# Optimization experiments

Measured on AMD Instinct MI355X. Metric: run time of the kernel, lower is better.

The kernel has to match this reference:

```python
import jax, jax.numpy as jnp
import numpy as np

B, K, F_DIM, H_DIM, HEADS = 512, 17, 256, 256, 4
N = B * K           # 8704 flattened nodes
E = 139264          # edges (avg degree 16)
NEG_SLOPE = 0.2


def setup_inputs() -> dict:
    key = jax.random.key(0)
    ks = jax.random.split(key, 12)
    s_in = 1.0 / np.sqrt(F_DIM)
    s_hid = 1.0 / np.sqrt(H_DIM)
    return {
        "kpt_feature": jax.random.normal(ks[0], (B, K, F_DIM), jnp.float32),
        "edge_index": jax.random.randint(ks[1], (2, E), 0, N, jnp.int64),
        # conv1: F_DIM -> HEADS x H_DIM, concat=False (mean)
        "W1": jax.random.normal(ks[2], (F_DIM, HEADS * H_DIM), jnp.float32) * s_in,
        "a_src1": jax.random.normal(ks[3], (HEADS, H_DIM), jnp.float32) * s_hid,
        "a_dst1": jax.random.normal(ks[4], (HEADS, H_DIM), jnp.float32) * s_hid,
        "b1": jnp.zeros((H_DIM,), jnp.float32),
        # conv2: H_DIM -> HEADS x F_DIM, concat=False (mean)
        "W2": jax.random.normal(ks[5], (H_DIM, HEADS * F_DIM), jnp.float32) * s_hid,
        "a_src2": jax.random.normal(ks[6], (HEADS, F_DIM), jnp.float32) * s_in,
        "a_dst2": jax.random.normal(ks[7], (HEADS, F_DIM), jnp.float32) * s_in,
        "b2": jnp.zeros((F_DIM,), jnp.float32),
    }


def gat_conv(x, src, dst, W, a_src, a_dst, bias):
    # x: [N, Fin]; src/dst: [E'] (self-loops included); W: [Fin, H*C]
    n = x.shape[0]
    heads, c = a_src.shape
    h = (x @ W).reshape(n, heads, c)                       # [N,H,C]
    alpha_src = jnp.einsum("nhc,hc->nh", h, a_src)         # [N,H]
    alpha_dst = jnp.einsum("nhc,hc->nh", h, a_dst)
    e = jax.nn.leaky_relu(alpha_src[src] + alpha_dst[dst], NEG_SLOPE)  # [E',H]
    # segment softmax over incoming edges of each destination node
    emax = jax.ops.segment_max(e, dst, num_segments=n)
    emax = jnp.where(jnp.isfinite(emax), emax, 0.0)
    ex = jnp.exp(e - emax[dst])
    denom = jax.ops.segment_sum(ex, dst, num_segments=n)
    alpha = ex / denom[dst]                                # [E',H]
    msg = alpha[:, :, None] * h[src]                       # [E',H,C]
    out = jax.ops.segment_sum(msg, dst, num_segments=n)    # [N,H,C]
    return out.mean(axis=1) + bias                         # concat=False -> mean


def reference(kpt_feature, edge_index, W1, a_src1, a_dst1, b1, W2, a_src2, a_dst2, b2):
    b, k, f = kpt_feature.shape
    n = b * k
    x = kpt_feature.reshape(n, f)
    loop = jnp.arange(n, dtype=edge_index.dtype)
    src = jnp.concatenate([edge_index[0], loop])  # PyG add_self_loops=True
    dst = jnp.concatenate([edge_index[1], loop])
    x = gat_conv(x, src, dst, W1, a_src1, a_dst1, b1)
    x = jax.nn.relu(x)
    x = gat_conv(x, src, dst, W2, a_src2, a_dst2, b2)
    return x.reshape(b, k, f)
```

## Files before the change

### kernel.cpp

```cpp
#include <hip/hip_runtime.h>
#include <hip/hip_fp16.h>
#include <math.h>

#define NNODES 8704
#define FDIM   256
#define HD     1024
#define NEDGE  139264
#define EPLUS  (NEDGE + NNODES)
#define NEG_SLOPE 0.2f
#define DEGCAP 64
#define LDSK   40

typedef _Float16 f16x8 __attribute__((ext_vector_type(8)));
typedef _Float16 f16x4 __attribute__((ext_vector_type(4)));
typedef _Float16 f16x2 __attribute__((ext_vector_type(2)));
typedef float    f32x4 __attribute__((ext_vector_type(4)));

__device__ __forceinline__ float lrelu(float v) { return v >= 0.f ? v : NEG_SLOPE * v; }

__global__ __launch_bounds__(256) void prep_pvec(const float* __restrict__ W1,
                                                 const float* __restrict__ as1,
                                                 const float* __restrict__ ad1,
                                                 const float* __restrict__ W2,
                                                 const float* __restrict__ as2,
                                                 const float* __restrict__ ad2,
                                                 float* __restrict__ pbuf,
                                                 int* __restrict__ cnt,
                                                 float* __restrict__ alphasB ) {
    const int b = blockIdx.x;
    const int t = threadIdx.x;
    for (int i = b * 256 + t; i < NNODES; i += 16 * 256) cnt[i] = 0;
    for (int i = b * 256 + t; i < NNODES * 8; i += 16 * 256) alphasB[i] = 0.f;
    __shared__ float a_sh[256];
    const int layer = b >> 3, sd = (b >> 2) & 1, h = b & 3;
    const float* W  = layer ? W2 : W1;
    const float* av = layer ? (sd ? ad2 : as2) : (sd ? ad1 : as1);
    a_sh[t] = av[h * 256 + t];
    __syncthreads();
    float acc = 0.f;
    const float* Wr = W + (size_t)t * 1024 + h * 256;
#pragma unroll 8
    for (int c = 0; c < 256; ++c) acc += Wr[c] * a_sh[c];
    pbuf[b * 256 + t] = acc;
}

__global__ __launch_bounds__(256) void prep_wcat(const float* __restrict__ W1,
                                                 const float* __restrict__ W2,
                                                 _Float16* __restrict__ Wc1,
                                                 _Float16* __restrict__ Wc2) {
    __shared__ float tile[32][33];
    const int k0 = blockIdx.x * 32, o0 = blockIdx.y * 32;
    const int layer = blockIdx.z >> 2, h = blockIdx.z & 3;
    const float* W = layer ? W2 : W1;
    _Float16* Wc   = layer ? Wc2 : Wc1;
    const int t = threadIdx.x;
#pragma unroll
    for (int p = 0; p < 4; ++p) {
        int e = t + p * 256; int kk = e >> 5, oo = e & 31;
        tile[kk][oo] = W[(size_t)(k0 + kk) * 1024 + h * 256 + o0 + oo];
    }
    __syncthreads();
#pragma unroll
    for (int p = 0; p < 4; ++p) {
        int e = t + p * 256; int oo = e >> 5, kk = e & 31;
        Wc[(size_t)(o0 + oo) * 1024 + h * 256 + k0 + kk] = (_Float16)tile[kk][oo];
    }
}

__global__ void edge_scatter(const int* __restrict__ ei, int* __restrict__ cnt,
                             int* __restrict__ csr) {
    int e = blockIdx.x * 256 + threadIdx.x;
    if (e >= EPLUS) return;
    int src, dst;
    if (e < NEDGE) { src = ei[e]; dst = ei[NEDGE + e]; }
    else           { src = dst = e - NEDGE; }
    int slot = atomicAdd(&cnt[dst], 1);
    if (slot < DEGCAP) csr[dst * DEGCAP + slot] = src;
}

__global__ __launch_bounds__(256) void alpha_dots(const float* __restrict__ xf,
                                                  _Float16* __restrict__ xh_out,
                                                  const float* __restrict__ p ,
                                                  float* __restrict__ asrc,
                                                  float* __restrict__ adst) {
    const int wave = threadIdx.x >> 6, l = threadIdx.x & 63;
    const int n = blockIdx.x * 4 + wave;
    float4 pv[8];
#pragma unroll
    for (int v = 0; v < 8; ++v) pv[v] = *(const float4*)(p + v * 256 + l * 4);
    float4 xv = *(const float4*)(xf + (size_t)n * 256 + l * 4);
    f16x4 hv = {(_Float16)xv.x, (_Float16)xv.y, (_Float16)xv.z, (_Float16)xv.w};
    *(f16x4*)(xh_out + (size_t)n * 256 + l * 4) = hv;
    float d[8];
#pragma unroll
    for (int v = 0; v < 8; ++v)
        d[v] = xv.x * pv[v].x + xv.y * pv[v].y + xv.z * pv[v].z + xv.w * pv[v].w;
#pragma unroll
    for (int off = 1; off <= 32; off <<= 1)
#pragma unroll
        for (int v = 0; v < 8; ++v) d[v] += __shfl_xor(d[v], off);
    if (l == 0) {
        *(float4*)(asrc + n * 4) = make_float4(d[0], d[1], d[2], d[3]);
        *(float4*)(adst + n * 4) = make_float4(d[4], d[5], d[6], d[7]);
    }
}

__global__ __launch_bounds__(256) void agg_gather(const _Float16* __restrict__ xh,
                                                  const int* __restrict__ cnt,
                                                  const int* __restrict__ csr,
                                                  const float* __restrict__ asrc,
                                                  const float* __restrict__ adst,
                                                  _Float16* __restrict__ y) {
    __shared__ float wbuf[DEGCAP][4];
    __shared__ int   sbuf[DEGCAP];
    __shared__ float sdinv[4];
    __shared__ float partial[4][4][256];

    const int n = blockIdx.x;
    const int t = threadIdx.x;
    int deg = cnt[n]; if (deg > DEGCAP) deg = DEGCAP;

    if (t < 64) {
        float4 ad = *(const float4*)(adst + n * 4);
        float w0 = 0.f, w1 = 0.f, w2 = 0.f, w3 = 0.f;
        if (t < deg) {
            int src = csr[n * DEGCAP + t];
            sbuf[t] = src;
            float4 as = *(const float4*)(asrc + src * 4);
            w0 = __expf(lrelu(as.x + ad.x));
            w1 = __expf(lrelu(as.y + ad.y));
            w2 = __expf(lrelu(as.z + ad.z));
            w3 = __expf(lrelu(as.w + ad.w));
            wbuf[t][0] = w0; wbuf[t][1] = w1; wbuf[t][2] = w2; wbuf[t][3] = w3;
        }
        float d0 = w0, d1 = w1, d2 = w2, d3 = w3;
#pragma unroll
        for (int off = 32; off >= 1; off >>= 1) {
            d0 += __shfl_xor(d0, off);
            d1 += __shfl_xor(d1, off);
            d2 += __shfl_xor(d2, off);
            d3 += __shfl_xor(d3, off);
        }
        if (t == 0) {
            sdinv[0] = 1.f / d0; sdinv[1] = 1.f / d1;
            sdinv[2] = 1.f / d2; sdinv[3] = 1.f / d3;
        }
    }
    __syncthreads();
    for (int i = t; i < deg * 4; i += 256) wbuf[i >> 2][i & 3] *= sdinv[i & 3];
    __syncthreads();

    const int g = t >> 6, l = t & 63;
    float acc[4][4] = {};
    for (int s = g; s < deg; s += 4) {
        int src = sbuf[s];
        float w0 = wbuf[s][0], w1 = wbuf[s][1], w2 = wbuf[s][2], w3 = wbuf[s][3];
        f16x4 xv = *(const f16x4*)(xh + (size_t)src * 256 + l * 4);
#pragma unroll
        for (int j = 0; j < 4; ++j) {
            float v = (float)xv[j];
            acc[j][0] += w0 * v; acc[j][1] += w1 * v;
            acc[j][2] += w2 * v; acc[j][3] += w3 * v;
        }
    }
#pragma unroll
    for (int j = 0; j < 4; ++j)
#pragma unroll
        for (int h = 0; h < 4; ++h) partial[g][h][l * 4 + j] = acc[j][h];
    __syncthreads();

    if (t < 128) {
#pragma unroll
        for (int h = 0; h < 4; ++h) {
            float v0 = partial[0][h][2*t]   + partial[1][h][2*t]   + partial[2][h][2*t]   + partial[3][h][2*t];
            float v1 = partial[0][h][2*t+1] + partial[1][h][2*t+1] + partial[2][h][2*t+1] + partial[3][h][2*t+1];
            f16x2 o = {(_Float16)v0, (_Float16)v1};
            *(f16x2*)(y + (size_t)n * 1024 + h * 256 + 2 * t) = o;
        }
    }
}

__global__ __launch_bounds__(256) void gemm_out(const _Float16* __restrict__ Y,
                                                const _Float16* __restrict__ Wcatt,
                                                const float* __restrict__ bias,
                                                const float* __restrict__ p2,
                                                _Float16* __restrict__ outH,
                                                float* __restrict__ outF,
                                                float* __restrict__ asrc2,
                                                float* __restrict__ adst2) {
    __shared__ __align__(16) _Float16 As[64 * LDSK];
    __shared__ __align__(16) _Float16 Bs[256 * LDSK];
    __shared__ float p2s[8 * 256];
    const int t    = threadIdx.x;
    const int lane = t & 63;
    const int wave = t >> 6;
    const int wwr = wave >> 1, wwc = wave & 1;
    const int bm = blockIdx.x * 64;
    const int l15 = lane & 15, kb = lane >> 4;

    f32x4 acc[2][8] = {};

    int a_off[2], b_off[8];
#pragma unroll
    for (int i = 0; i < 2; ++i) a_off[i] = (wwr * 32 + i * 16 + l15) * LDSK + kb * 8;
#pragma unroll
    for (int j = 0; j < 8; ++j) b_off[j] = (wwc * 128 + j * 16 + l15) * LDSK + kb * 8;

    for (int k0 = 0; k0 < 1024; k0 += 32) {
        if (k0) __syncthreads();
        {
            int row = t >> 2, g = t & 3;
            f16x8 v = *(const f16x8*)(Y + (size_t)(bm + row) * 1024 + k0 + g * 8);
            *(f16x8*)(&As[row * LDSK + g * 8]) = v;
        }
#pragma unroll
        for (int p = 0; p < 4; ++p) {
            int e = t + p * 256;
            int row = e >> 2, g = e & 3;
            f16x8 v = *(const f16x8*)(Wcatt + (size_t)row * 1024 + k0 + g * 8);
            *(f16x8*)(&Bs[row * LDSK + g * 8]) = v;
        }
        __syncthreads();

        f16x8 af[2], bf[8];
#pragma unroll
        for (int i = 0; i < 2; ++i) af[i] = *(const f16x8*)(&As[a_off[i]]);
#pragma unroll
        for (int j = 0; j < 8; ++j) bf[j] = *(const f16x8*)(&Bs[b_off[j]]);
#pragma unroll
        for (int i = 0; i < 2; ++i)
#pragma unroll
            for (int j = 0; j < 8; ++j)
                acc[i][j] = __builtin_amdgcn_mfma_f32_16x16x32_f16(af[i], bf[j], acc[i][j], 0, 0, 0);
    }

    if (p2) {
#pragma unroll
        for (int v = 0; v < 8; ++v) p2s[v * 256 + t] = p2[v * 256 + t];
    }
    __syncthreads();

#pragma unroll
    for (int i = 0; i < 2; ++i)
#pragma unroll
        for (int q = 0; q < 4; ++q) {
            int row = bm + wwr * 32 + i * 16 + kb * 4 + q;
            float rv[8];
#pragma unroll
            for (int j = 0; j < 8; ++j) {
                int col = wwc * 128 + j * 16 + l15;
                float r = 0.25f * acc[i][j][q] + bias[col];
                rv[j] = r;
                if (outH) outH[(size_t)row * 256 + col] = (_Float16)fmaxf(r, 0.f);
                else      outF[(size_t)row * 256 + col] = r;
            }
            if (p2) {
#pragma unroll
                for (int v = 0; v < 8; ++v) {
                    float ps = 0.f;
#pragma unroll
                    for (int j = 0; j < 8; ++j) {
                        int col = wwc * 128 + j * 16 + l15;
                        ps += fmaxf(rv[j], 0.f) * p2s[v * 256 + col];
                    }
#pragma unroll
                    for (int off = 1; off <= 8; off <<= 1) ps += __shfl_xor(ps, off);
                    if (l15 == 0) {
                        if (v < 4) atomicAdd(&asrc2[row * 4 + v], ps);
                        else       atomicAdd(&adst2[row * 4 + (v - 4)], ps);
                    }
                }
            }
        }
}

extern "C" void kernel_launch(void* const* d_in, const int* in_sizes, int n_in,
                              void* d_out, int out_size, void* d_ws, size_t ws_size,
                              hipStream_t stream) {
    const float* x0  = (const float*)d_in[0];
    const int*   ei  = (const int*)d_in[1];
    const float* W1  = (const float*)d_in[2];
    const float* as1 = (const float*)d_in[3];
    const float* ad1 = (const float*)d_in[4];
    const float* b1  = (const float*)d_in[5];
    const float* W2  = (const float*)d_in[6];
    const float* as2 = (const float*)d_in[7];
    const float* ad2 = (const float*)d_in[8];
    const float* b2  = (const float*)d_in[9];
    float* out = (float*)d_out;

    char* w = (char*)d_ws;
    _Float16* y   = (_Float16*)w; w += (size_t)NNODES * HD * 2;
    _Float16* x0h = (_Float16*)w; w += (size_t)NNODES * FDIM * 2;
    _Float16* x1h = (_Float16*)w; w += (size_t)NNODES * FDIM * 2;
    _Float16* Wc1 = (_Float16*)w; w += (size_t)256 * 1024 * 2;
    _Float16* Wc2 = (_Float16*)w; w += (size_t)256 * 1024 * 2;
    float* pbuf   = (float*)w;    w += 16 * 256 * 4;
    float* asrcA  = (float*)w;    w += NNODES * 4 * 4;
    float* adstA  = (float*)w;    w += NNODES * 4 * 4;
    float* alphasB = (float*)w;   w += NNODES * 8 * 4;
    float* asrcB  = alphasB;
    float* adstB  = alphasB + NNODES * 4;
    int* cnt      = (int*)w;      w += NNODES * 4;
    int* csr      = (int*)w;      w += (size_t)NNODES * DEGCAP * 4;

    const dim3 eb((EPLUS + 255) / 256);
    const dim3 wcat_grid(8, 8, 8);

    prep_pvec<<<16, 256, 0, stream>>>(W1, as1, ad1, W2, as2, ad2, pbuf, cnt, alphasB);
    prep_wcat<<<wcat_grid, 256, 0, stream>>>(W1, W2, Wc1, Wc2);
    edge_scatter<<<eb, 256, 0, stream>>>(ei, cnt, csr);

    alpha_dots<<<NNODES / 4, 256, 0, stream>>>(x0, x0h, pbuf, asrcA, adstA);
    agg_gather<<<NNODES, 256, 0, stream>>>(x0h, cnt, csr, asrcA, adstA, y);
    gemm_out<<<NNODES / 64, 256, 0, stream>>>(y, Wc1, b1, pbuf + 8 * 256, x1h, nullptr, asrcB, adstB);

    agg_gather<<<NNODES, 256, 0, stream>>>(x1h, cnt, csr, asrcB, adstB, y);
    gemm_out<<<NNODES / 64, 256, 0, stream>>>(y, Wc2, b2, nullptr, nullptr, out, nullptr, nullptr);
}
```

Measured before the change: 149.4 us.

## Split output GEMM across column tiles to increase block count

Change the output GEMM tiling from a 64x256 tile per block to 64x64 tiles over a 2D grid, with a deeper K step of 64 and padded LDS rows. This raises the number of blocks so more compute units are occupied. The fused attention-score epilogue now accumulates partial dot products per column block through atomics. The trade-off is redundant reloading of the Y activation tile across the four column blocks and lower MFMA work per LDS load.

```diff
diff --git a/kernel.cpp b/kernel.cpp
--- a/kernel.cpp
+++ b/kernel.cpp
@@ -10,6 +10,7 @@
 #define NEG_SLOPE 0.2f
 #define DEGCAP 64
 #define LDSK   40
+#define LDSK2  72
 
 typedef _Float16 f16x8 __attribute__((ext_vector_type(8)));
 typedef _Float16 f16x4 __attribute__((ext_vector_type(4)));
@@ -188,55 +189,60 @@
                                                 float* __restrict__ outF,
                                                 float* __restrict__ asrc2,
                                                 float* __restrict__ adst2) {
-    __shared__ __align__(16) _Float16 As[64 * LDSK];
-    __shared__ __align__(16) _Float16 Bs[256 * LDSK];
-    __shared__ float p2s[8 * 256];
+    __shared__ __align__(16) _Float16 As[64 * LDSK2];
+    __shared__ __align__(16) _Float16 Bs[64 * LDSK2];
+    __shared__ float p2s[8 * 64];
     const int t    = threadIdx.x;
     const int lane = t & 63;
     const int wave = t >> 6;
     const int wwr = wave >> 1, wwc = wave & 1;
     const int bm = blockIdx.x * 64;
+    const int bn = blockIdx.y * 64;
     const int l15 = lane & 15, kb = lane >> 4;
 
-    f32x4 acc[2][8] = {};
-
-    int a_off[2], b_off[8];
-#pragma unroll
-    for (int i = 0; i < 2; ++i) a_off[i] = (wwr * 32 + i * 16 + l15) * LDSK + kb * 8;
-#pragma unroll
-    for (int j = 0; j < 8; ++j) b_off[j] = (wwc * 128 + j * 16 + l15) * LDSK + kb * 8;
-
-    for (int k0 = 0; k0 < 1024; k0 += 32) {
+    f32x4 acc[2][2] = {};
+
+    int a_off[2], b_off[2];
+#pragma unroll
+    for (int i = 0; i < 2; ++i) a_off[i] = (wwr * 32 + i * 16 + l15) * LDSK2 + kb * 8;
+#pragma unroll
+    for (int j = 0; j < 2; ++j) b_off[j] = (wwc * 32 + j * 16 + l15) * LDSK2 + kb * 8;
+
+    for (int k0 = 0; k0 < 1024; k0 += 64) {
         if (k0) __syncthreads();
-        {
-            int row = t >> 2, g = t & 3;
-            f16x8 v = *(const f16x8*)(Y + (size_t)(bm + row) * 1024 + k0 + g * 8);
-            *(f16x8*)(&As[row * LDSK + g * 8]) = v;
-        }
-#pragma unroll
-        for (int p = 0; p < 4; ++p) {
+#pragma unroll
+        for (int p = 0; p < 2; ++p) {
             int e = t + p * 256;
-            int row = e >> 2, g = e & 3;
-            f16x8 v = *(const f16x8*)(Wcatt + (size_t)row * 1024 + k0 + g * 8);
-            *(f16x8*)(&Bs[row * LDSK + g * 8]) = v;
+            int row = e >> 3, g = e & 7;
+            f16x8 va = *(const f16x8*)(Y + (size_t)(bm + row) * 1024 + k0 + g * 8);
+            *(f16x8*)(&As[row * LDSK2 + g * 8]) = va;
+            f16x8 vb = *(const f16x8*)(Wcatt + (size_t)(bn + row) * 1024 + k0 + g * 8);
+            *(f16x8*)(&Bs[row * LDSK2 + g * 8]) = vb;
         }
         __syncthreads();
 
-        f16x8 af[2], bf[8];
-#pragma unroll
-        for (int i = 0; i < 2; ++i) af[i] = *(const f16x8*)(&As[a_off[i]]);
-#pragma unroll
-        for (int j = 0; j < 8; ++j) bf[j] = *(const f16x8*)(&Bs[b_off[j]]);
-#pragma unroll
-        for (int i = 0; i < 2; ++i)
-#pragma unroll
-            for (int j = 0; j < 8; ++j)
-                acc[i][j] = __builtin_amdgcn_mfma_f32_16x16x32_f16(af[i], bf[j], acc[i][j], 0, 0, 0);
+#pragma unroll
+        for (int ks = 0; ks < 2; ++ks) {
+            f16x8 af[2], bf[2];
+#pragma unroll
+            for (int i = 0; i < 2; ++i) af[i] = *(const f16x8*)(&As[a_off[i] + ks * 32]);
+#pragma unroll
+            for (int j = 0; j < 2; ++j) bf[j] = *(const f16x8*)(&Bs[b_off[j] + ks * 32]);
+#pragma unroll
+            for (int i = 0; i < 2; ++i)
+#pragma unroll
+                for (int j = 0; j < 2; ++j)
+                    acc[i][j] = __builtin_amdgcn_mfma_f32_16x16x32_f16(af[i], bf[j], acc[i][j], 0, 0, 0);
+        }
     }
 
     if (p2) {
 #pragma unroll
-        for (int v = 0; v < 8; ++v) p2s[v * 256 + t] = p2[v * 256 + t];
+        for (int p = 0; p < 2; ++p) {
+            int e = t + p * 256;
+            int v = e >> 6, c = e & 63;
+            p2s[e] = p2[v * 256 + bn + c];
+        }
     }
     __syncthreads();
 
@@ -245,23 +251,23 @@
 #pragma unroll
         for (int q = 0; q < 4; ++q) {
             int row = bm + wwr * 32 + i * 16 + kb * 4 + q;
-            float rv[8];
-#pragma unroll
-            for (int j = 0; j < 8; ++j) {
-                int col = wwc * 128 + j * 16 + l15;
-                float r = 0.25f * acc[i][j][q] + bias[col];
+            float rv[2];
+#pragma unroll
+            for (int j = 0; j < 2; ++j) {
+                int cl = wwc * 32 + j * 16 + l15;
+                float r = 0.25f * acc[i][j][q] + bias[bn + cl];
                 rv[j] = r;
-                if (outH) outH[(size_t)row * 256 + col] = (_Float16)fmaxf(r, 0.f);
-                else      outF[(size_t)row * 256 + col] = r;
+                if (outH) outH[(size_t)row * 256 + bn + cl] = (_Float16)fmaxf(r, 0.f);
+                else      outF[(size_t)row * 256 + bn + cl] = r;
             }
             if (p2) {
 #pragma unroll
                 for (int v = 0; v < 8; ++v) {
                     float ps = 0.f;
 #pragma unroll
-                    for (int j = 0; j < 8; ++j) {
-                        int col = wwc * 128 + j * 16 + l15;
-                        ps += fmaxf(rv[j], 0.f) * p2s[v * 256 + col];
+                    for (int j = 0; j < 2; ++j) {
+                        int cl = wwc * 32 + j * 16 + l15;
+                        ps += fmaxf(rv[j], 0.f) * p2s[v * 64 + cl];
                     }
 #pragma unroll
                     for (int off = 1; off <= 8; off <<= 1) ps += __shfl_xor(ps, off);
@@ -306,6 +312,7 @@
 
     const dim3 eb((EPLUS + 255) / 256);
     const dim3 wcat_grid(8, 8, 8);
+    const dim3 gemm_grid(NNODES / 64, 4);
 
     prep_pvec<<<16, 256, 0, stream>>>(W1, as1, ad1, W2, as2, ad2, pbuf, cnt, alphasB);
     prep_wcat<<<wcat_grid, 256, 0, stream>>>(W1, W2, Wc1, Wc2);
@@ -313,8 +320,8 @@
 
     alpha_dots<<<NNODES / 4, 256, 0, stream>>>(x0, x0h, pbuf, asrcA, adstA);
     agg_gather<<<NNODES, 256, 0, stream>>>(x0h, cnt, csr, asrcA, adstA, y);
-    gemm_out<<<NNODES / 64, 256, 0, stream>>>(y, Wc1, b1, pbuf + 8 * 256, x1h, nullptr, asrcB, adstB);
+    gemm_out<<<gemm_grid, 256, 0, stream>>>(y, Wc1, b1, pbuf + 8 * 256, x1h, nullptr, asrcB, adstB);
 
     agg_gather<<<NNODES, 256, 0, stream>>>(x1h, cnt, csr, asrcB, adstB, y);
-    gemm_out<<<NNODES / 64, 256, 0, stream>>>(y, Wc2, b2, nullptr, nullptr, out, nullptr, nullptr);
-}
+    gemm_out<<<gemm_grid, 256, 0, stream>>>(y, Wc2, b2, nullptr, nullptr, out, nullptr, nullptr);
+}
```

After: 172.0 us. 1.15x slower.

## Merge prep kernels and remap aggregation to one wave per node

Applied to the files above, without the earlier changes.

Fuses the pvec and weight-transpose prep kernels into one launch, and the edge scatter with the alpha dot products into another, which cuts the launch count from eight to six. The aggregation kernel now gives each destination node a single wave instead of a whole block. Softmax weights and source indices are broadcast with shuffles, which removes the shared-memory buffers, the barriers and the cross-wave reduction. The trade-off is that each wave walks all edges of its node serially, so per-node gather latency is less hidden and the loads are less parallel per node.

```diff
diff --git a/kernel.cpp b/kernel.cpp
--- a/kernel.cpp
+++ b/kernel.cpp
@@ -3,105 +3,111 @@
 #include <math.h>
 
 #define NNODES 8704
-#define FDIM   256
-#define HD     1024
 #define NEDGE  139264
 #define EPLUS  (NEDGE + NNODES)
 #define NEG_SLOPE 0.2f
 #define DEGCAP 64
 #define LDSK   40
 
+#define NB_PV  16
+#define NB_WC  512
+#define NB_SC  ((EPLUS + 255) / 256)
+#define NB_AL  (NNODES / 4)
+
 typedef _Float16 f16x8 __attribute__((ext_vector_type(8)));
 typedef _Float16 f16x4 __attribute__((ext_vector_type(4)));
-typedef _Float16 f16x2 __attribute__((ext_vector_type(2)));
 typedef float    f32x4 __attribute__((ext_vector_type(4)));
 
 __device__ __forceinline__ float lrelu(float v) { return v >= 0.f ? v : NEG_SLOPE * v; }
 
-__global__ __launch_bounds__(256) void prep_pvec(const float* __restrict__ W1,
-                                                 const float* __restrict__ as1,
-                                                 const float* __restrict__ ad1,
-                                                 const float* __restrict__ W2,
-                                                 const float* __restrict__ as2,
-                                                 const float* __restrict__ ad2,
-                                                 float* __restrict__ pbuf,
-                                                 int* __restrict__ cnt,
-                                                 float* __restrict__ alphasB ) {
+__global__ __launch_bounds__(256) void prep_all(const float* __restrict__ W1,
+                                                const float* __restrict__ as1,
+                                                const float* __restrict__ ad1,
+                                                const float* __restrict__ W2,
+                                                const float* __restrict__ as2,
+                                                const float* __restrict__ ad2,
+                                                float* __restrict__ pbuf,
+                                                int* __restrict__ cnt,
+                                                float* __restrict__ alphasB,
+                                                _Float16* __restrict__ Wc1,
+                                                _Float16* __restrict__ Wc2) {
+    __shared__ float tile[32][33];
     const int b = blockIdx.x;
     const int t = threadIdx.x;
-    for (int i = b * 256 + t; i < NNODES; i += 16 * 256) cnt[i] = 0;
-    for (int i = b * 256 + t; i < NNODES * 8; i += 16 * 256) alphasB[i] = 0.f;
-    __shared__ float a_sh[256];
-    const int layer = b >> 3, sd = (b >> 2) & 1, h = b & 3;
-    const float* W  = layer ? W2 : W1;
-    const float* av = layer ? (sd ? ad2 : as2) : (sd ? ad1 : as1);
-    a_sh[t] = av[h * 256 + t];
-    __syncthreads();
-    float acc = 0.f;
-    const float* Wr = W + (size_t)t * 1024 + h * 256;
+    if (b < NB_PV) {
+        for (int i = b * 256 + t; i < NNODES; i += NB_PV * 256) cnt[i] = 0;
+        for (int i = b * 256 + t; i < NNODES * 8; i += NB_PV * 256) alphasB[i] = 0.f;
+        float* a_sh = &tile[0][0];
+        const int layer = b >> 3, sd = (b >> 2) & 1, h = b & 3;
+        const float* W  = layer ? W2 : W1;
+        const float* av = layer ? (sd ? ad2 : as2) : (sd ? ad1 : as1);
+        a_sh[t] = av[h * 256 + t];
+        __syncthreads();
+        float acc = 0.f;
+        const float* Wr = W + (size_t)t * 1024 + h * 256;
 #pragma unroll 8
-    for (int c = 0; c < 256; ++c) acc += Wr[c] * a_sh[c];
-    pbuf[b * 256 + t] = acc;
-}
-
-__global__ __launch_bounds__(256) void prep_wcat(const float* __restrict__ W1,
-                                                 const float* __restrict__ W2,
-                                                 _Float16* __restrict__ Wc1,
-                                                 _Float16* __restrict__ Wc2) {
-    __shared__ float tile[32][33];
-    const int k0 = blockIdx.x * 32, o0 = blockIdx.y * 32;
-    const int layer = blockIdx.z >> 2, h = blockIdx.z & 3;
-    const float* W = layer ? W2 : W1;
-    _Float16* Wc   = layer ? Wc2 : Wc1;
+        for (int c = 0; c < 256; ++c) acc += Wr[c] * a_sh[c];
+        pbuf[b * 256 + t] = acc;
+    } else {
+        const int idx = b - NB_PV;
+        const int k0 = (idx & 7) * 32, o0 = ((idx >> 3) & 7) * 32;
+        const int z = idx >> 6;
+        const int layer = z >> 2, h = z & 3;
+        const float* W = layer ? W2 : W1;
+        _Float16* Wc   = layer ? Wc2 : Wc1;
+#pragma unroll
+        for (int p = 0; p < 4; ++p) {
+            int e = t + p * 256; int kk = e >> 5, oo = e & 31;
+            tile[kk][oo] = W[(size_t)(k0 + kk) * 1024 + h * 256 + o0 + oo];
+        }
+        __syncthreads();
+#pragma unroll
+        for (int p = 0; p < 4; ++p) {
+            int e = t + p * 256; int oo = e >> 5, kk = e & 31;
+            Wc[(size_t)(o0 + oo) * 1024 + h * 256 + k0 + kk] = (_Float16)tile[kk][oo];
+        }
+    }
+}
+
+__global__ __launch_bounds__(256) void scatter_alpha(const int* __restrict__ ei,
+                                                     int* __restrict__ cnt,
+                                                     int* __restrict__ csr,
+                                                     const float* __restrict__ xf,
+                                                     _Float16* __restrict__ xh_out,
+                                                     const float* __restrict__ p ,
+                                                     float* __restrict__ asrc,
+                                                     float* __restrict__ adst) {
+    const int b = blockIdx.x;
     const int t = threadIdx.x;
-#pragma unroll
-    for (int p = 0; p < 4; ++p) {
-        int e = t + p * 256; int kk = e >> 5, oo = e & 31;
-        tile[kk][oo] = W[(size_t)(k0 + kk) * 1024 + h * 256 + o0 + oo];
-    }
-    __syncthreads();
-#pragma unroll
-    for (int p = 0; p < 4; ++p) {
-        int e = t + p * 256; int oo = e >> 5, kk = e & 31;
-        Wc[(size_t)(o0 + oo) * 1024 + h * 256 + k0 + kk] = (_Float16)tile[kk][oo];
-    }
-}
-
-__global__ void edge_scatter(const int* __restrict__ ei, int* __restrict__ cnt,
-                             int* __restrict__ csr) {
-    int e = blockIdx.x * 256 + threadIdx.x;
-    if (e >= EPLUS) return;
-    int src, dst;
-    if (e < NEDGE) { src = ei[e]; dst = ei[NEDGE + e]; }
-    else           { src = dst = e - NEDGE; }
-    int slot = atomicAdd(&cnt[dst], 1);
-    if (slot < DEGCAP) csr[dst * DEGCAP + slot] = src;
-}
-
-__global__ __launch_bounds__(256) void alpha_dots(const float* __restrict__ xf,
-                                                  _Float16* __restrict__ xh_out,
-                                                  const float* __restrict__ p ,
-                                                  float* __restrict__ asrc,
-                                                  float* __restrict__ adst) {
-    const int wave = threadIdx.x >> 6, l = threadIdx.x & 63;
-    const int n = blockIdx.x * 4 + wave;
-    float4 pv[8];
-#pragma unroll
-    for (int v = 0; v < 8; ++v) pv[v] = *(const float4*)(p + v * 256 + l * 4);
-    float4 xv = *(const float4*)(xf + (size_t)n * 256 + l * 4);
-    f16x4 hv = {(_Float16)xv.x, (_Float16)xv.y, (_Float16)xv.z, (_Float16)xv.w};
-    *(f16x4*)(xh_out + (size_t)n * 256 + l * 4) = hv;
-    float d[8];
-#pragma unroll
-    for (int v = 0; v < 8; ++v)
-        d[v] = xv.x * pv[v].x + xv.y * pv[v].y + xv.z * pv[v].z + xv.w * pv[v].w;
-#pragma unroll
-    for (int off = 1; off <= 32; off <<= 1)
-#pragma unroll
-        for (int v = 0; v < 8; ++v) d[v] += __shfl_xor(d[v], off);
-    if (l == 0) {
-        *(float4*)(asrc + n * 4) = make_float4(d[0], d[1], d[2], d[3]);
-        *(float4*)(adst + n * 4) = make_float4(d[4], d[5], d[6], d[7]);
+    if (b < NB_SC) {
+        int e = b * 256 + t;
+        if (e >= EPLUS) return;
+        int src, dst;
+        if (e < NEDGE) { src = ei[e]; dst = ei[NEDGE + e]; }
+        else           { src = dst = e - NEDGE; }
+        int slot = atomicAdd(&cnt[dst], 1);
+        if (slot < DEGCAP) csr[dst * DEGCAP + slot] = src;
+    } else {
+        const int wave = t >> 6, l = t & 63;
+        const int n = (b - NB_SC) * 4 + wave;
+        float4 pv[8];
+#pragma unroll
+        for (int v = 0; v < 8; ++v) pv[v] = *(const float4*)(p + v * 256 + l * 4);
+        float4 xv = *(const float4*)(xf + (size_t)n * 256 + l * 4);
+        f16x4 hv = {(_Float16)xv.x, (_Float16)xv.y, (_Float16)xv.z, (_Float16)xv.w};
+        *(f16x4*)(xh_out + (size_t)n * 256 + l * 4) = hv;
+        float d[8];
+#pragma unroll
+        for (int v = 0; v < 8; ++v)
+            d[v] = xv.x * pv[v].x + xv.y * pv[v].y + xv.z * pv[v].z + xv.w * pv[v].w;
+#pragma unroll
+        for (int off = 1; off <= 32; off <<= 1)
+#pragma unroll
+            for (int v = 0; v < 8; ++v) d[v] += __shfl_xor(d[v], off);
+        if (l == 0) {
+            *(float4*)(asrc + n * 4) = make_float4(d[0], d[1], d[2], d[3]);
+            *(float4*)(adst + n * 4) = make_float4(d[4], d[5], d[6], d[7]);
+        }
     }
 }
 
@@ -111,72 +117,49 @@
                                                   const float* __restrict__ asrc,
                                                   const float* __restrict__ adst,
                                                   _Float16* __restrict__ y) {
-    __shared__ float wbuf[DEGCAP][4];
-    __shared__ int   sbuf[DEGCAP];
-    __shared__ float sdinv[4];
-    __shared__ float partial[4][4][256];
-
-    const int n = blockIdx.x;
-    const int t = threadIdx.x;
+    const int w = threadIdx.x >> 6, l = threadIdx.x & 63;
+    const int n = blockIdx.x * 4 + w;
     int deg = cnt[n]; if (deg > DEGCAP) deg = DEGCAP;
 
-    if (t < 64) {
-        float4 ad = *(const float4*)(adst + n * 4);
-        float w0 = 0.f, w1 = 0.f, w2 = 0.f, w3 = 0.f;
-        if (t < deg) {
-            int src = csr[n * DEGCAP + t];
-            sbuf[t] = src;
-            float4 as = *(const float4*)(asrc + src * 4);
-            w0 = __expf(lrelu(as.x + ad.x));
-            w1 = __expf(lrelu(as.y + ad.y));
-            w2 = __expf(lrelu(as.z + ad.z));
-            w3 = __expf(lrelu(as.w + ad.w));
-            wbuf[t][0] = w0; wbuf[t][1] = w1; wbuf[t][2] = w2; wbuf[t][3] = w3;
-        }
-        float d0 = w0, d1 = w1, d2 = w2, d3 = w3;
-#pragma unroll
-        for (int off = 32; off >= 1; off >>= 1) {
-            d0 += __shfl_xor(d0, off);
-            d1 += __shfl_xor(d1, off);
-            d2 += __shfl_xor(d2, off);
-            d3 += __shfl_xor(d3, off);
-        }
-        if (t == 0) {
-            sdinv[0] = 1.f / d0; sdinv[1] = 1.f / d1;
-            sdinv[2] = 1.f / d2; sdinv[3] = 1.f / d3;
-        }
-    }
-    __syncthreads();
-    for (int i = t; i < deg * 4; i += 256) wbuf[i >> 2][i & 3] *= sdinv[i & 3];
-    __syncthreads();
-
-    const int g = t >> 6, l = t & 63;
+    float4 ad = *(const float4*)(adst + n * 4);
+    int src_l = 0;
+    float w0 = 0.f, w1 = 0.f, w2 = 0.f, w3 = 0.f;
+    if (l < deg) {
+        src_l = csr[n * DEGCAP + l];
+        float4 as = *(const float4*)(asrc + src_l * 4);
+        w0 = __expf(lrelu(as.x + ad.x));
+        w1 = __expf(lrelu(as.y + ad.y));
+        w2 = __expf(lrelu(as.z + ad.z));
+        w3 = __expf(lrelu(as.w + ad.w));
+    }
+    float d0 = w0, d1 = w1, d2 = w2, d3 = w3;
+#pragma unroll
+    for (int off = 32; off >= 1; off >>= 1) {
+        d0 += __shfl_xor(d0, off);
+        d1 += __shfl_xor(d1, off);
+        d2 += __shfl_xor(d2, off);
+        d3 += __shfl_xor(d3, off);
+    }
+    w0 /= d0; w1 /= d1; w2 /= d2; w3 /= d3;
+
     float acc[4][4] = {};
-    for (int s = g; s < deg; s += 4) {
-        int src = sbuf[s];
-        float w0 = wbuf[s][0], w1 = wbuf[s][1], w2 = wbuf[s][2], w3 = wbuf[s][3];
+    for (int s = 0; s < deg; ++s) {
+        int src = __shfl(src_l, s);
+        float u0 = __shfl(w0, s), u1 = __shfl(w1, s);
+        float u2 = __shfl(w2, s), u3 = __shfl(w3, s);
         f16x4 xv = *(const f16x4*)(xh + (size_t)src * 256 + l * 4);
 #pragma unroll
         for (int j = 0; j < 4; ++j) {
             float v = (float)xv[j];
-            acc[j][0] += w0 * v; acc[j][1] += w1 * v;
-            acc[j][2] += w2 * v; acc[j][3] += w3 * v;
-        }
-    }
-#pragma unroll
-    for (int j = 0; j < 4; ++j)
-#pragma unroll
-        for (int h = 0; h < 4; ++h) partial[g][h][l * 4 + j] = acc[j][h];
-    __syncthreads();
-
-    if (t < 128) {
-#pragma unroll
-        for (int h = 0; h < 4; ++h) {
-            float v0 = partial[0][h][2*t]   + partial[1][h][2*t]   + partial[2][h][2*t]   + partial[3][h][2*t];
-            float v1 = partial[0][h][2*t+1] + partial[1][h][2*t+1] + partial[2][h][2*t+1] + partial[3][h][2*t+1];
-            f16x2 o = {(_Float16)v0, (_Float16)v1};
-            *(f16x2*)(y + (size_t)n * 1024 + h * 256 + 2 * t) = o;
-        }
+            acc[j][0] += u0 * v; acc[j][1] += u1 * v;
+            acc[j][2] += u2 * v; acc[j][3] += u3 * v;
+        }
+    }
+#pragma unroll
+    for (int h = 0; h < 4; ++h) {
+        f16x4 pv = {(_Float16)acc[0][h], (_Float16)acc[1][h],
+                    (_Float16)acc[2][h], (_Float16)acc[3][h]};
+        *(f16x4*)(y + (size_t)n * 1024 + h * 256 + l * 4) = pv;
     }
 }
 
@@ -290,9 +273,9 @@
     float* out = (float*)d_out;
 
     char* w = (char*)d_ws;
-    _Float16* y   = (_Float16*)w; w += (size_t)NNODES * HD * 2;
-    _Float16* x0h = (_Float16*)w; w += (size_t)NNODES * FDIM * 2;
-    _Float16* x1h = (_Float16*)w; w += (size_t)NNODES * FDIM * 2;
+    _Float16* y   = (_Float16*)w; w += (size_t)NNODES * 1024 * 2;
+    _Float16* x0h = (_Float16*)w; w += (size_t)NNODES * 256 * 2;
+    _Float16* x1h = (_Float16*)w; w += (size_t)NNODES * 256 * 2;
     _Float16* Wc1 = (_Float16*)w; w += (size_t)256 * 1024 * 2;
     _Float16* Wc2 = (_Float16*)w; w += (size_t)256 * 1024 * 2;
     float* pbuf   = (float*)w;    w += 16 * 256 * 4;
@@ -304,17 +287,13 @@
     int* cnt      = (int*)w;      w += NNODES * 4;
     int* csr      = (int*)w;      w += (size_t)NNODES * DEGCAP * 4;
 
-    const dim3 eb((EPLUS + 255) / 256);
-    const dim3 wcat_grid(8, 8, 8);
-
-    prep_pvec<<<16, 256, 0, stream>>>(W1, as1, ad1, W2, as2, ad2, pbuf, cnt, alphasB);
-    prep_wcat<<<wcat_grid, 256, 0, stream>>>(W1, W2, Wc1, Wc2);
-    edge_scatter<<<eb, 256, 0, stream>>>(ei, cnt, csr);
-
-    alpha_dots<<<NNODES / 4, 256, 0, stream>>>(x0, x0h, pbuf, asrcA, adstA);
-    agg_gather<<<NNODES, 256, 0, stream>>>(x0h, cnt, csr, asrcA, adstA, y);
+    prep_all<<<NB_PV + NB_WC, 256, 0, stream>>>(W1, as1, ad1, W2, as2, ad2,
+                                                pbuf, cnt, alphasB, Wc1, Wc2);
+    scatter_alpha<<<NB_SC + NB_AL, 256, 0, stream>>>(ei, cnt, csr, x0, x0h, pbuf, asrcA, adstA);
+
+    agg_gather<<<NNODES / 4, 256, 0, stream>>>(x0h, cnt, csr, asrcA, adstA, y);
     gemm_out<<<NNODES / 64, 256, 0, stream>>>(y, Wc1, b1, pbuf + 8 * 256, x1h, nullptr, asrcB, adstB);
 
-    agg_gather<<<NNODES, 256, 0, stream>>>(x1h, cnt, csr, asrcB, adstB, y);
+    agg_gather<<<NNODES / 4, 256, 0, stream>>>(x1h, cnt, csr, asrcB, adstB, y);
     gemm_out<<<NNODES / 64, 256, 0, stream>>>(y, Wc2, b2, nullptr, nullptr, out, nullptr, nullptr);
 }
```

After: 142.3 us. 4.8% less time.
